# Performance work log

Measured on AMD Instinct MI355X. Metric: run time of the kernel, lower is better.

Reference implementation:

```python
import jax, jax.numpy as jnp
import numpy as np

B, N, C = 64, 197, 768
H = 12
N_TOK = 118
CUTOFF = 0.15


def setup_inputs() -> dict:
    key = jax.random.key(0)
    ks = jax.random.split(key, 6)
    s = 0.02
    return {
        "x": jax.random.normal(ks[0], (B, N, C), jnp.float32),
        "ln1_w": jnp.ones((C,), jnp.float32),
        "ln1_b": jnp.zeros((C,), jnp.float32),
        "qkv_w": jax.random.normal(ks[1], (3 * C, C), jnp.float32) * s,
        "proj_w": jax.random.normal(ks[2], (C, C), jnp.float32) * s,
        "proj_b": jnp.zeros((C,), jnp.float32),
        "gamma1": jnp.ones((C,), jnp.float32),
        "ln2_w": jnp.ones((C,), jnp.float32),
        "ln2_b": jnp.zeros((C,), jnp.float32),
        "fc1_w": jax.random.normal(ks[3], (4 * C, C), jnp.float32) * s,
        "fc1_b": jnp.zeros((4 * C,), jnp.float32),
        "fc2_w": jax.random.normal(ks[4], (C, 4 * C), jnp.float32) * s,
        "fc2_b": jnp.zeros((C,), jnp.float32),
        "gamma2": jnp.ones((C,), jnp.float32),
    }


def _ln(x, w, b, eps=1e-5):
    m = x.mean(-1, keepdims=True)
    v = ((x - m) ** 2).mean(-1, keepdims=True)
    return (x - m) / jnp.sqrt(v + eps) * w + b


def _attention(x, qkv_w, proj_w, proj_b):
    Bx, Nx, Cx = x.shape
    dh = Cx // H
    qkv = x @ qkv_w.T                                    # [B,N,3C]
    qk = qkv[:, :, : 2 * Cx].reshape(Bx, Nx, 2, H, dh).transpose(2, 0, 3, 1, 4)
    q, k = qk[0], qk[1]                                  # [B,H,N,dh]
    v = qkv[:, :, 2 * Cx :].reshape(Bx, Nx, H, dh).transpose(0, 2, 1, 3)
    attn = jax.nn.softmax((q * dh ** -0.5) @ k.transpose(0, 1, 3, 2), axis=-1)  # [B,H,N,N]
    out = (attn @ v).transpose(0, 2, 1, 3).reshape(Bx, Nx, Cx)
    return out @ proj_w.T + proj_b, attn


def _selector(x, attn, n_tokens, cutoff):
    # attention-weighted scores
    cls_aw = attn[:, :, 1:, 0].mean(-1)[..., None]        # [B,H,1]
    cls_attn = (attn[:, :, 0, 1:] * cls_aw).mean(1)       # [B,N-1]
    img_aw = attn[:, :, 0, 0][..., None]                  # [B,H,1]
    img_attn = (attn[:, :, 1:, 1:].mean(2) * img_aw).mean(1)
    token_attn = cls_attn + img_attn                      # [B,N-1]
    # FFT low-frequency-energy score (detached in original)
    img_token = jax.lax.stop_gradient(x[:, 1:].astype(jnp.float32).transpose(0, 2, 1))  # [B,C,N-1]
    f = jnp.fft.fft(img_token, axis=-1)
    amp = jnp.abs(f)
    pha = jnp.angle(f)
    L = img_token.shape[-1]
    d0 = (L * cutoff / 2.0) ** 2
    m0 = (L - 1) / 2.0
    grid = jnp.arange(L, dtype=jnp.float32)
    kernel = 1.0 - jnp.exp(-((grid - m0) ** 2) / (2.0 * d0))  # high-pass notch
    amp = amp * kernel
    f2 = amp * jnp.cos(pha) + 1j * amp * jnp.sin(pha)
    tok = jnp.fft.ifft(f2, axis=-1)                       # [B,C,N-1] complex
    token_lfe = jnp.abs(tok).sum(1) / jnp.abs(img_token).sum(1).mean(-1)[..., None]
    scores = token_lfe * token_attn                        # [B,N-1]
    _, idx = jax.lax.top_k(scores, n_tokens)               # [B,n_tokens]
    Cx = x.shape[-1]
    sav = jnp.take_along_axis(x[:, 1:], idx[:, :, None], axis=1)  # [B,n_tokens,C]
    return jnp.concatenate([x[:, 0:1], sav], axis=1)


def reference(x, ln1_w, ln1_b, qkv_w, proj_w, proj_b, gamma1,
              ln2_w, ln2_b, fc1_w, fc1_b, fc2_w, fc2_b, gamma2):
    x_msa, attn = _attention(_ln(x, ln1_w, ln1_b), qkv_w, proj_w, proj_b)
    x = gamma1 * x_msa + x
    x = _selector(x, attn, N_TOK, CUTOFF)                 # [B,1+N_TOK,C]
    h = _ln(x, ln2_w, ln2_b)
    h = jax.nn.gelu(h @ fc1_w.T + fc1_b, approximate=False)
    h = h @ fc2_w.T + fc2_b
    return gamma2 * h + x
```

## Files before the change

kernel.cpp:

```cpp
#include <hip/hip_runtime.h>
#include <math.h>

#define NTOK 197
#define NIMG 196
#define CDIM 768
#define NHEAD 12
#define HD 64
#define BATCH 64
#define NSEL 118
#define ROWS_FULL (BATCH*NTOK)
#define ROWS_SEL  (BATCH*(NSEL+1))

typedef short bf16x8 __attribute__((ext_vector_type(8)));
typedef float f32x4  __attribute__((ext_vector_type(4)));

#define GLDS(g, l) __builtin_amdgcn_global_load_lds( \
    (const __attribute__((address_space(1))) void*)(g), \
    (__attribute__((address_space(3))) void*)(l), 16, 0, 0)

__device__ __forceinline__ unsigned short f2bf(float f){
  union { float f; unsigned u; } v; v.f = f;
  unsigned r = v.u + 0x7FFF + ((v.u >> 16) & 1);
  return (unsigned short)(r >> 16);
}
__device__ __forceinline__ float bf2f(unsigned short h){
  union { unsigned u; float f; } v; v.u = ((unsigned)h) << 16; return v.f;
}

template<int OUT>
__global__ __launch_bounds__(256) void ln_kernel(
    const float* __restrict__ x, const float* __restrict__ w,
    const float* __restrict__ b, void* __restrict__ outv)
{
  const int row = blockIdx.x;
  const int t = threadIdx.x;
  const float* xr = x + (size_t)row * CDIM;
  float v0 = xr[t], v1 = xr[t+256], v2 = xr[t+512];
  float s = v0 + v1 + v2;
  __shared__ float red[4], red2[4];
  #pragma unroll
  for (int o=32;o>0;o>>=1) s += __shfl_down(s,o);
  if ((t&63)==0) red[t>>6] = s;
  __syncthreads();
  const float mean = (red[0]+red[1]+red[2]+red[3]) / 768.0f;
  const float d0=v0-mean, d1=v1-mean, d2=v2-mean;
  float vs = d0*d0 + d1*d1 + d2*d2;
  #pragma unroll
  for (int o=32;o>0;o>>=1) vs += __shfl_down(vs,o);
  if ((t&63)==0) red2[t>>6] = vs;
  __syncthreads();
  const float var = (red2[0]+red2[1]+red2[2]+red2[3]) / 768.0f;
  const float rstd = 1.0f / sqrtf(var + 1e-5f);
  const float o0 = d0*rstd*w[t]     + b[t];
  const float o1 = d1*rstd*w[t+256] + b[t+256];
  const float o2 = d2*rstd*w[t+512] + b[t+512];
  if (OUT == 0){
    float* orow = (float*)outv + (size_t)row * CDIM;
    orow[t] = o0; orow[t+256] = o1; orow[t+512] = o2;
  } else {
    unsigned short* orow = (unsigned short*)outv + (size_t)row * CDIM;
    orow[t] = f2bf(o0); orow[t+256] = f2bf(o1); orow[t+512] = f2bf(o2);
  }
}

__global__ __launch_bounds__(256) void ln_split3_kernel(
    const float* __restrict__ x, const float* __restrict__ w,
    const float* __restrict__ b, unsigned short* __restrict__ dst, size_t plane)
{
  const int row = blockIdx.x;
  const int t = threadIdx.x;
  const float* xr = x + (size_t)row * CDIM;
  float v0 = xr[t], v1 = xr[t+256], v2 = xr[t+512];
  float s = v0 + v1 + v2;
  __shared__ float red[4], red2[4];
  #pragma unroll
  for (int o=32;o>0;o>>=1) s += __shfl_down(s,o);
  if ((t&63)==0) red[t>>6] = s;
  __syncthreads();
  const float mean = (red[0]+red[1]+red[2]+red[3]) / 768.0f;
  const float d0=v0-mean, d1=v1-mean, d2=v2-mean;
  float vs = d0*d0 + d1*d1 + d2*d2;
  #pragma unroll
  for (int o=32;o>0;o>>=1) vs += __shfl_down(vs,o);
  if ((t&63)==0) red2[t>>6] = vs;
  __syncthreads();
  const float var = (red2[0]+red2[1]+red2[2]+red2[3]) / 768.0f;
  const float rstd = 1.0f / sqrtf(var + 1e-5f);
  const float ov[3] = { d0*rstd*w[t]     + b[t],
                        d1*rstd*w[t+256] + b[t+256],
                        d2*rstd*w[t+512] + b[t+512] };
  #pragma unroll
  for (int e=0;e<3;e++){
    const int col = t + e*256;
    const float f = ov[e];
    const unsigned short p0 = f2bf(f);
    const float r1 = f - bf2f(p0);
    const unsigned short p1 = f2bf(r1);
    const unsigned short p2 = f2bf(r1 - bf2f(p1));
    dst[(size_t)row*CDIM + col]             = p0;
    dst[plane + (size_t)row*CDIM + col]     = p1;
    dst[2*plane + (size_t)row*CDIM + col]   = p2;
  }
}

__global__ __launch_bounds__(256) void cvt_bf16_kernel(
    const float* __restrict__ src, unsigned short* __restrict__ dst, int n4)
{
  const int i = blockIdx.x*256 + threadIdx.x;
  if (i < n4){
    const float4 v = *(const float4*)(src + (size_t)i*4);
    dst[(size_t)i*4+0] = f2bf(v.x); dst[(size_t)i*4+1] = f2bf(v.y);
    dst[(size_t)i*4+2] = f2bf(v.z); dst[(size_t)i*4+3] = f2bf(v.w);
  }
}

__global__ __launch_bounds__(192) void cvt3_kernel(
    const float* __restrict__ w, unsigned short* __restrict__ W3, int K)
{
  const int n = blockIdx.x, t = threadIdx.x;
  const float4 v = *(const float4*)(w + (size_t)n*K + t*4);
  ushort4 hi, lo;
  hi.x = f2bf(v.x); lo.x = f2bf(v.x - bf2f(hi.x));
  hi.y = f2bf(v.y); lo.y = f2bf(v.y - bf2f(hi.y));
  hi.z = f2bf(v.z); lo.z = f2bf(v.z - bf2f(hi.z));
  hi.w = f2bf(v.w); lo.w = f2bf(v.w - bf2f(hi.w));
  *(ushort4*)(W3 + (size_t)n*2*K + t*4)     = hi;
  *(ushort4*)(W3 + (size_t)n*2*K + K + t*4) = lo;
}

__global__ __launch_bounds__(256) void cvt_split3_kernel(
    const float* __restrict__ src, unsigned short* __restrict__ dst,
    int n4, size_t plane)
{
  const int i = blockIdx.x*256 + threadIdx.x;
  if (i >= n4) return;
  const float4 v = *(const float4*)(src + (size_t)i*4);
  const float f[4] = {v.x, v.y, v.z, v.w};
  unsigned short p0[4], p1[4], p2[4];
  #pragma unroll
  for (int q=0;q<4;q++){
    p0[q] = f2bf(f[q]);
    const float r1 = f[q] - bf2f(p0[q]);
    p1[q] = f2bf(r1);
    const float r2 = r1 - bf2f(p1[q]);
    p2[q] = f2bf(r2);
  }
  *(ushort4*)(dst + (size_t)i*4)           = make_ushort4(p0[0],p0[1],p0[2],p0[3]);
  *(ushort4*)(dst + plane + (size_t)i*4)   = make_ushort4(p1[0],p1[1],p1[2],p1[3]);
  *(ushort4*)(dst + 2*plane + (size_t)i*4) = make_ushort4(p2[0],p2[1],p2[2],p2[3]);
}

__global__ __launch_bounds__(256) void gemm_f32_kernel(
    const float* __restrict__ A, const float* __restrict__ W,
    float* __restrict__ out, int M, int N, int K)
{
  __shared__ float As[16][132];
  __shared__ float Bs[16][132];
  const int t  = threadIdx.x;
  const int tx = t & 15, ty = t >> 4;
  const int m0 = blockIdx.x * 128, n0 = blockIdx.y * 128;
  const int lr = t >> 2, lc = (t & 3) << 2;
  float acc[2][2][4][4] = {{{{0.f}}}};
  const float4 z4 = make_float4(0.f,0.f,0.f,0.f);
  const int rowA0 = m0 + lr, rowA1 = m0 + 64 + lr;
  const size_t strA0 = (size_t)rowA0 * K, strA1 = (size_t)rowA1 * K;
  const size_t strW0 = (size_t)(n0+lr) * K, strW1 = (size_t)(n0+64+lr) * K;
  for (int k0=0; k0<K; k0+=16){
    float4 a0 = (rowA0 < M) ? *(const float4*)(A + strA0 + k0 + lc) : z4;
    float4 a1 = (rowA1 < M) ? *(const float4*)(A + strA1 + k0 + lc) : z4;
    float4 w0 = *(const float4*)(W + strW0 + k0 + lc);
    float4 w1 = *(const float4*)(W + strW1 + k0 + lc);
    __syncthreads();
    As[lc+0][lr]=a0.x; As[lc+1][lr]=a0.y; As[lc+2][lr]=a0.z; As[lc+3][lr]=a0.w;
    As[lc+0][64+lr]=a1.x; As[lc+1][64+lr]=a1.y; As[lc+2][64+lr]=a1.z; As[lc+3][64+lr]=a1.w;
    Bs[lc+0][lr]=w0.x; Bs[lc+1][lr]=w0.y; Bs[lc+2][lr]=w0.z; Bs[lc+3][lr]=w0.w;
    Bs[lc+0][64+lr]=w1.x; Bs[lc+1][64+lr]=w1.y; Bs[lc+2][64+lr]=w1.z; Bs[lc+3][64+lr]=w1.w;
    __syncthreads();
    #pragma unroll
    for (int k=0;k<16;k++){
      const float4 av0 = *(const float4*)&As[k][ty*4];
      const float4 av1 = *(const float4*)&As[k][64+ty*4];
      const float4 bv0 = *(const float4*)&Bs[k][tx*4];
      const float4 bv1 = *(const float4*)&Bs[k][64+tx*4];
      const float ar[2][4] = {{av0.x,av0.y,av0.z,av0.w},{av1.x,av1.y,av1.z,av1.w}};
      const float br[2][4] = {{bv0.x,bv0.y,bv0.z,bv0.w},{bv1.x,bv1.y,bv1.z,bv1.w}};
      #pragma unroll
      for (int ri=0;ri<2;ri++)
        #pragma unroll
        for (int i=0;i<4;i++)
          #pragma unroll
          for (int ci=0;ci<2;ci++)
            #pragma unroll
            for (int j=0;j<4;j++)
              acc[ri][ci][i][j] = fmaf(ar[ri][i], br[ci][j], acc[ri][ci][i][j]);
    }
  }
  #pragma unroll
  for (int ri=0;ri<2;ri++){
    #pragma unroll
    for (int i=0;i<4;i++){
      const int row = m0 + ri*64 + ty*4 + i;
      if (row >= M) continue;
      #pragma unroll
      for (int ci=0;ci<2;ci++){
        const int col = n0 + ci*64 + tx*4;
        *(float4*)(out + (size_t)row*N + col) =
          make_float4(acc[ri][ci][i][0],acc[ri][ci][i][1],acc[ri][ci][i][2],acc[ri][ci][i][3]);
      }
    }
  }
}

template<int EPI>
__global__ __launch_bounds__(256) void mfma_gemm_kernel(
    const unsigned short* __restrict__ A, const unsigned short* __restrict__ W,
    const float* __restrict__ bias, const float* __restrict__ gamma,
    const float* __restrict__ resid, void* __restrict__ outv,
    int M, int N, int K)
{
  __shared__ __align__(16) unsigned short As[128*64];
  __shared__ __align__(16) unsigned short Bs[128*64];
  const int t = threadIdx.x;
  const int w = t >> 6, lane = t & 63;
  const int m0 = blockIdx.x * 128, n0 = blockIdx.y * 128;
  const int wr = w >> 1, wc = w & 1;
  f32x4 acc[4][4];
  #pragma unroll
  for (int i=0;i<4;i++)
    #pragma unroll
    for (int j=0;j<4;j++){ acc[i][j][0]=0.f; acc[i][j][1]=0.f; acc[i][j][2]=0.f; acc[i][j][3]=0.f; }

  const int srow = lane >> 3;
  const int slot = lane & 7;
  const int scol = (slot ^ srow) * 8;
  const int rloc0 = w*32;
  const int fr = lane & 15;
  const int kg = lane >> 4;

  for (int k0 = 0; k0 < K; k0 += 64){
    __syncthreads();
    #pragma unroll
    for (int tt = 0; tt < 4; tt++){
      const int rl = rloc0 + tt*8;
      const int ra = rl + srow;
      GLDS(A + (size_t)(m0 + ra)*K + k0 + scol, As + rl*64);
      GLDS(W + (size_t)(n0 + ra)*K + k0 + scol, Bs + rl*64);
    }
    __syncthreads();
    #pragma unroll
    for (int ksub = 0; ksub < 2; ksub++){
      bf16x8 a[4], b[4];
      const int kbyte = ksub*64 + kg*16;
      #pragma unroll
      for (int mi=0; mi<4; mi++){
        const int ar = wr*64 + mi*16 + fr;
        a[mi] = *(const bf16x8*)(As + ar*64 + ((kbyte ^ ((ar&7)<<4)) >> 1));
      }
      #pragma unroll
      for (int ni=0; ni<4; ni++){
        const int br = wc*64 + ni*16 + fr;
        b[ni] = *(const bf16x8*)(Bs + br*64 + ((kbyte ^ ((br&7)<<4)) >> 1));
      }
      #pragma unroll
      for (int mi=0; mi<4; mi++)
        #pragma unroll
        for (int ni=0; ni<4; ni++)
          acc[mi][ni] = __builtin_amdgcn_mfma_f32_16x16x32_bf16(a[mi], b[ni], acc[mi][ni], 0, 0, 0);
    }
  }

  const int cL = lane & 15, rL = lane >> 4;
  #pragma unroll
  for (int mi=0; mi<4; mi++){
    #pragma unroll
    for (int ni=0; ni<4; ni++){
      const int col = n0 + wc*64 + ni*16 + cL;
      const int rowb = m0 + wr*64 + mi*16 + rL*4;
      const float bb = bias[col];
      #pragma unroll
      for (int r=0; r<4; r++){
        const int row = rowb + r;
        if (row >= M) continue;
        float v = acc[mi][ni][r] + bb;
        if (EPI == 2){
          v = 0.5f*v*(1.0f + erff(v*0.7071067811865475f));
          ((unsigned short*)outv)[(size_t)row*N + col] = f2bf(v);
        } else {
          v = gamma[col]*v + resid[(size_t)row*N + col];
          ((float*)outv)[(size_t)row*N + col] = v;
        }
      }
    }
  }
}

__global__ __launch_bounds__(512) void mfma_gemm6w_kernel(
    const unsigned short* __restrict__ A3, const unsigned short* __restrict__ W3,
    float* __restrict__ out, int M, int N, int K, size_t planeA, size_t planeW,
    int gx)
{
  __shared__ __align__(16) unsigned short As[3][64*64];
  __shared__ __align__(16) unsigned short Ws[256*64];
  const int nwg = gridDim.x;
  const int q8 = nwg >> 3, r8 = nwg & 7;
  const int xcd = blockIdx.x & 7, lid = blockIdx.x >> 3;
  const int swz = (xcd < r8) ? (xcd*(q8+1) + lid) : (r8*(q8+1) + (xcd-r8)*q8 + lid);
  const int bx = swz % gx, by = swz / gx;

  const int t = threadIdx.x;
  const int w = t >> 6, lane = t & 63;
  const int m0 = bx * 64, n0 = by * 256;
  const int wr = w >> 2, wc = w & 3;
  f32x4 acc[2][4];
  #pragma unroll
  for (int i=0;i<2;i++)
    #pragma unroll
    for (int j=0;j<4;j++){ acc[i][j][0]=0.f; acc[i][j][1]=0.f; acc[i][j][2]=0.f; acc[i][j][3]=0.f; }

  const int srow = lane >> 3;
  const int slot = lane & 7;
  const int scol = (slot ^ srow) * 8;
  const int aloc = w*8;
  const int wloc = w*32;
  const int fr = lane & 15;
  const int kg = lane >> 4;

  #define SEGW(NA)                                                            \
    _Pragma("unroll")                                                         \
    for (int ksub = 0; ksub < 2; ksub++){                                     \
      const int kbyte = ksub*64 + kg*16;                                      \
      bf16x8 b[4];                                                            \
      _Pragma("unroll")                                                       \
      for (int ni=0; ni<4; ni++){                                             \
        const int br = wc*64 + ni*16 + fr;                                    \
        b[ni] = *(const bf16x8*)(Ws + br*64 + ((kbyte ^ ((br&7)<<4)) >> 1));  \
      }                                                                       \
      _Pragma("unroll")                                                       \
      for (int p=0; p<NA; p++){                                               \
        bf16x8 a[2];                                                          \
        _Pragma("unroll")                                                     \
        for (int mi=0; mi<2; mi++){                                           \
          const int ar = wr*32 + mi*16 + fr;                                  \
          a[mi] = *(const bf16x8*)(As[p] + ar*64 + ((kbyte ^ ((ar&7)<<4)) >> 1)); \
        }                                                                     \
        _Pragma("unroll")                                                     \
        for (int mi=0; mi<2; mi++)                                            \
          _Pragma("unroll")                                                   \
          for (int ni=0; ni<4; ni++)                                          \
            acc[mi][ni] = __builtin_amdgcn_mfma_f32_16x16x32_bf16(a[mi], b[ni], acc[mi][ni], 0, 0, 0); \
      }                                                                       \
    }

  #define STAGE_W(P)                                                          \
    _Pragma("unroll")                                                         \
    for (int tt=0; tt<4; tt++){                                               \
      const int rl = wloc + tt*8;                                             \
      GLDS(W3 + (size_t)(P)*planeW + (size_t)(n0+rl+srow)*K + k0 + scol, Ws + rl*64); \
    }

  for (int k0 = 0; k0 < K; k0 += 64){
    __syncthreads();
    #pragma unroll
    for (int p=0; p<3; p++)
      GLDS(A3 + (size_t)p*planeA + (size_t)(m0+aloc+srow)*K + k0 + scol, As[p] + aloc*64);
    STAGE_W(0)
    __syncthreads();
    SEGW(3)
    __syncthreads();
    STAGE_W(1)
    __syncthreads();
    SEGW(2)
    __syncthreads();
    STAGE_W(2)
    __syncthreads();
    SEGW(1)
  }
  #undef SEGW
  #undef STAGE_W

  const int cL = lane & 15, rL = lane >> 4;
  #pragma unroll
  for (int mi=0; mi<2; mi++){
    #pragma unroll
    for (int ni=0; ni<4; ni++){
      const int col = n0 + wc*64 + ni*16 + cL;
      const int rowb = m0 + wr*32 + mi*16 + rL*4;
      #pragma unroll
      for (int r=0; r<4; r++){
        const int row = rowb + r;
        if (row >= M) continue;
        out[(size_t)row*N + col] = acc[mi][ni][r];
      }
    }
  }
}

__global__ __launch_bounds__(512) void mfma_proj3_kernel(
    const unsigned short* __restrict__ A, const unsigned short* __restrict__ W,
    const float* __restrict__ bias, const float* __restrict__ gamma,
    const float* __restrict__ resid, float* __restrict__ out,
    int M, int N, int K, int gx)
{
  __shared__ __align__(16) unsigned short Ah[64*64], Al[64*64];
  __shared__ __align__(16) unsigned short Ws[256*64];
  const int nwg = gridDim.x;
  const int q8 = nwg >> 3, r8 = nwg & 7;
  const int xcd = blockIdx.x & 7, lid = blockIdx.x >> 3;
  const int swz = (xcd < r8) ? (xcd*(q8+1) + lid) : (r8*(q8+1) + (xcd-r8)*q8 + lid);
  const int bx = swz % gx, by = swz / gx;

  const int t = threadIdx.x;
  const int w = t >> 6, lane = t & 63;
  const int m0 = bx * 64, n0 = by * 256;
  const int wr = w >> 2, wc = w & 3;
  const int lda = 2*K;
  f32x4 acc[2][4];
  #pragma unroll
  for (int i=0;i<2;i++)
    #pragma unroll
    for (int j=0;j<4;j++){ acc[i][j][0]=0.f; acc[i][j][1]=0.f; acc[i][j][2]=0.f; acc[i][j][3]=0.f; }

  const int srow = lane >> 3;
  const int slot = lane & 7;
  const int scol = (slot ^ srow) * 8;
  const int aloc = w*8;
  const int wloc = w*32;
  const int fr = lane & 15;
  const int kg = lane >> 4;

  #define PSEG(NA)                                                            \
    _Pragma("unroll")                                                         \
    for (int ksub = 0; ksub < 2; ksub++){                                     \
      const int kbyte = ksub*64 + kg*16;                                      \
      bf16x8 b[4];                                                            \
      _Pragma("unroll")                                                       \
      for (int ni=0; ni<4; ni++){                                             \
        const int br = wc*64 + ni*16 + fr;                                    \
        b[ni] = *(const bf16x8*)(Ws + br*64 + ((kbyte ^ ((br&7)<<4)) >> 1));  \
      }                                                                       \
      _Pragma("unroll")                                                       \
      for (int mi=0; mi<2; mi++){                                             \
        const int ar = wr*32 + mi*16 + fr;                                    \
        const int ao = ar*64 + ((kbyte ^ ((ar&7)<<4)) >> 1);                  \
        bf16x8 ah = *(const bf16x8*)(Ah + ao);                                \
        _Pragma("unroll")                                                     \
        for (int ni=0; ni<4; ni++)                                            \
          acc[mi][ni] = __builtin_amdgcn_mfma_f32_16x16x32_bf16(ah, b[ni], acc[mi][ni], 0, 0, 0); \
        if (NA > 1){                                                          \
          bf16x8 al = *(const bf16x8*)(Al + ao);                              \
          _Pragma("unroll")                                                   \
          for (int ni=0; ni<4; ni++)                                          \
            acc[mi][ni] = __builtin_amdgcn_mfma_f32_16x16x32_bf16(al, b[ni], acc[mi][ni], 0, 0, 0); \
        }                                                                     \
      }                                                                       \
    }

  for (int k0 = 0; k0 < K; k0 += 64){
    __syncthreads();
    {
      const size_t abase = (size_t)(m0+aloc+srow)*lda + k0 + scol;
      GLDS(A + abase,     Ah + aloc*64);
      GLDS(A + abase + K, Al + aloc*64);
    }
    #pragma unroll
    for (int tt=0; tt<4; tt++){
      const int rl = wloc + tt*8;
      GLDS(W + (size_t)(n0+rl+srow)*lda + k0 + scol, Ws + rl*64);
    }
    __syncthreads();
    PSEG(2)
    __syncthreads();
    #pragma unroll
    for (int tt=0; tt<4; tt++){
      const int rl = wloc + tt*8;
      GLDS(W + (size_t)(n0+rl+srow)*lda + K + k0 + scol, Ws + rl*64);
    }
    __syncthreads();
    PSEG(1)
  }
  #undef PSEG

  const int cL = lane & 15, rL = lane >> 4;
  #pragma unroll
  for (int mi=0; mi<2; mi++){
    #pragma unroll
    for (int ni=0; ni<4; ni++){
      const int col = n0 + wc*64 + ni*16 + cL;
      const int rowb = m0 + wr*32 + mi*16 + rL*4;
      const float bb = bias[col];
      const float gg = gamma[col];
      #pragma unroll
      for (int r=0; r<4; r++){
        const int row = rowb + r;
        if (row >= M) continue;
        out[(size_t)row*N + col] = gg*(acc[mi][ni][r] + bb) + resid[(size_t)row*N + col];
      }
    }
  }
}

__global__ __launch_bounds__(256) void attn_stats_kernel(
    const float* __restrict__ qkv, double* __restrict__ mbuf, double* __restrict__ lbuf)
{
  __shared__ float Kt[NTOK][HD];
  __shared__ double q0s[HD];
  __shared__ float m0sh;
  __shared__ double red[4];
  const int bh = blockIdx.x;
  const int b = bh / NHEAD, h = bh % NHEAD;
  const float* basep = qkv + (size_t)b*NTOK*2304 + h*HD;
  for (int li=threadIdx.x; li<NTOK*16; li+=256){
    const int r = li >> 4, c4 = (li & 15) << 2;
    *(float4*)&Kt[r][c4] = *(const float4*)(basep + (size_t)r*2304 + 768 + c4);
  }
  if (threadIdx.x < 16){
    const float4 t4 = *(const float4*)(basep + threadIdx.x*4);
    q0s[threadIdx.x*4+0] = (double)t4.x*0.125; q0s[threadIdx.x*4+1] = (double)t4.y*0.125;
    q0s[threadIdx.x*4+2] = (double)t4.z*0.125; q0s[threadIdx.x*4+3] = (double)t4.w*0.125;
  }
  __syncthreads();
  const int i = threadIdx.x;
  if (i < NTOK){
    float4 q[16];
    #pragma unroll
    for (int dd=0; dd<16; dd++){
      float4 tq = *(const float4*)(basep + (size_t)i*2304 + dd*4);
      q[dd] = make_float4(tq.x*0.125f, tq.y*0.125f, tq.z*0.125f, tq.w*0.125f);
    }
    float m = -INFINITY, l = 0.f;
    for (int j=0;j<NTOK;j++){
      float s = 0.f;
      #pragma unroll
      for (int dd=0;dd<16;dd++){
        const float4 kk = *(const float4*)&Kt[j][dd*4];
        s = fmaf(q[dd].x,kk.x,s); s = fmaf(q[dd].y,kk.y,s);
        s = fmaf(q[dd].z,kk.z,s); s = fmaf(q[dd].w,kk.w,s);
      }
      const float mn = fmaxf(m, s);
      l = l*expf(m-mn) + expf(s-mn);
      m = mn;
    }
    mbuf[bh*NTOK+i] = (double)m;
    if (i > 0) lbuf[bh*NTOK+i] = (double)(1.0f/l);
    if (i == 0) m0sh = m;
  }
  __syncthreads();
  double e = 0.0;
  if (i < NTOK){
    double s64 = 0.0;
    #pragma unroll
    for (int d=0; d<HD; d++) s64 = fma(q0s[d], (double)Kt[i][d], s64);
    e = exp(s64 - (double)m0sh);
  }
  #pragma unroll
  for (int o=32;o>0;o>>=1) e += __shfl_down(e,o);
  if ((i&63)==0) red[i>>6] = e;
  __syncthreads();
  if (i==0) lbuf[bh*NTOK] = 1.0/(red[0]+red[1]+red[2]+red[3]);
}

__global__ __launch_bounds__(256) void attn_pv_kernel(
    const float* __restrict__ qkv, const double* __restrict__ mbuf,
    const double* __restrict__ lbuf, unsigned short* __restrict__ msa3)
{
  __shared__ float Kt[NTOK][HD];
  __shared__ float Vt[NTOK][HD];
  const int bh = blockIdx.x;
  const int b = bh / NHEAD, h = bh % NHEAD;
  const float* basep = qkv + (size_t)b*NTOK*2304 + h*HD;
  for (int li=threadIdx.x; li<NTOK*16; li+=256){
    const int r = li >> 4, c4 = (li & 15) << 2;
    *(float4*)&Kt[r][c4] = *(const float4*)(basep + (size_t)r*2304 +  768 + c4);
    *(float4*)&Vt[r][c4] = *(const float4*)(basep + (size_t)r*2304 + 1536 + c4);
  }
  __syncthreads();
  const int i = threadIdx.x;
  if (i >= NTOK) return;
  float4 q[16];
  #pragma unroll
  for (int dd=0; dd<16; dd++){
    float4 tq = *(const float4*)(basep + (size_t)i*2304 + dd*4);
    q[dd] = make_float4(tq.x*0.125f, tq.y*0.125f, tq.z*0.125f, tq.w*0.125f);
  }
  const float m    = (float)mbuf[bh*NTOK + i];
  const float linv = (float)lbuf[bh*NTOK + i];
  float4 o[16];
  #pragma unroll
  for (int dd=0;dd<16;dd++) o[dd] = make_float4(0.f,0.f,0.f,0.f);
  for (int j=0;j<NTOK;j++){
    float s = 0.f;
    #pragma unroll
    for (int dd=0;dd<16;dd++){
      const float4 kk = *(const float4*)&Kt[j][dd*4];
      s = fmaf(q[dd].x,kk.x,s); s = fmaf(q[dd].y,kk.y,s);
      s = fmaf(q[dd].z,kk.z,s); s = fmaf(q[dd].w,kk.w,s);
    }
    const float p = expf(s - m) * linv;
    #pragma unroll
    for (int dd=0;dd<16;dd++){
      const float4 vv = *(const float4*)&Vt[j][dd*4];
      o[dd].x = fmaf(p,vv.x,o[dd].x); o[dd].y = fmaf(p,vv.y,o[dd].y);
      o[dd].z = fmaf(p,vv.z,o[dd].z); o[dd].w = fmaf(p,vv.w,o[dd].w);
    }
  }
  unsigned short* orow = msa3 + ((size_t)b*NTOK + i)*1536 + h*HD;
  #pragma unroll
  for (int dd=0;dd<16;dd++){
    const float4 v = o[dd];
    ushort4 hi, lo;
    hi.x = f2bf(v.x); lo.x = f2bf(v.x - bf2f(hi.x));
    hi.y = f2bf(v.y); lo.y = f2bf(v.y - bf2f(hi.y));
    hi.z = f2bf(v.z); lo.z = f2bf(v.z - bf2f(hi.z));
    hi.w = f2bf(v.w); lo.w = f2bf(v.w - bf2f(hi.w));
    *(ushort4*)(orow + dd*4)       = hi;
    *(ushort4*)(orow + 768 + dd*4) = lo;
  }
}

__global__ __launch_bounds__(256) void attn_sel_kernel(
    const float* __restrict__ qkv, const double* __restrict__ mbuf,
    const double* __restrict__ lbuf, double* __restrict__ ta_part)
{
  __shared__ float Qt[NTOK][HD];
  __shared__ double q0s[HD];
  __shared__ float msf[NTOK], lsf[NTOK];
  __shared__ double m0d, l0inv;
  __shared__ double sh_cs0, sh_r00;
  const int bh = blockIdx.x;
  const int b = bh / NHEAD, h = bh % NHEAD;
  const float* basep = qkv + (size_t)b*NTOK*2304 + h*HD;
  for (int li=threadIdx.x; li<NTOK*16; li+=256){
    const int r = li >> 4, c4 = (li & 15) << 2;
    float4 tq = *(const float4*)(basep + (size_t)r*2304 + c4);
    Qt[r][c4+0]=tq.x*0.125f; Qt[r][c4+1]=tq.y*0.125f;
    Qt[r][c4+2]=tq.z*0.125f; Qt[r][c4+3]=tq.w*0.125f;
  }
  if (threadIdx.x < 16){
    const float4 t4 = *(const float4*)(basep + threadIdx.x*4);
    q0s[threadIdx.x*4+0] = (double)t4.x*0.125; q0s[threadIdx.x*4+1] = (double)t4.y*0.125;
    q0s[threadIdx.x*4+2] = (double)t4.z*0.125; q0s[threadIdx.x*4+3] = (double)t4.w*0.125;
  }
  for (int li=threadIdx.x; li<NTOK; li+=256){
    msf[li] = (float)mbuf[bh*NTOK+li];
    lsf[li] = (float)lbuf[bh*NTOK+li];
  }
  if (threadIdx.x == 0){ m0d = mbuf[bh*NTOK]; l0inv = lbuf[bh*NTOK]; }
  __syncthreads();
  const int j = threadIdx.x;
  double colsum = 0.0, row0 = 0.0;
  if (j < NTOK){
    float4 kreg[16];
    #pragma unroll
    for (int dd=0;dd<16;dd++) kreg[dd] = *(const float4*)(basep + (size_t)j*2304 + 768 + dd*4);
    {
      double s64 = 0.0;
      #pragma unroll
      for (int dd=0;dd<16;dd++){
        s64 = fma(q0s[dd*4+0], (double)kreg[dd].x, s64);
        s64 = fma(q0s[dd*4+1], (double)kreg[dd].y, s64);
        s64 = fma(q0s[dd*4+2], (double)kreg[dd].z, s64);
        s64 = fma(q0s[dd*4+3], (double)kreg[dd].w, s64);
      }
      row0 = exp(s64 - m0d) * l0inv;
    }
    for (int i2=1;i2<NTOK;i2++){
      float s = 0.f;
      #pragma unroll
      for (int dd=0;dd<16;dd++){
        const float4 qq = *(const float4*)&Qt[i2][dd*4];
        s = fmaf(qq.x,kreg[dd].x,s); s = fmaf(qq.y,kreg[dd].y,s);
        s = fmaf(qq.z,kreg[dd].z,s); s = fmaf(qq.w,kreg[dd].w,s);
      }
      colsum += (double)(expf(s - msf[i2]) * lsf[i2]);
    }
  }
  if (j == 0){ sh_cs0 = colsum; sh_r00 = row0; }
  __syncthreads();
  if (j >= 1 && j < NTOK){
    ta_part[(size_t)bh*NIMG + (j-1)] = row0 * (sh_cs0 / 196.0) + (colsum / 196.0) * sh_r00;
  }
}

__global__ __launch_bounds__(256) void reduce_ta_kernel(
    const double* __restrict__ ta_part, double* __restrict__ token_attn)
{
  const int b = blockIdx.x, j = threadIdx.x;
  if (j < NIMG){
    double s = 0.0;
    for (int h=0; h<NHEAD; h++) s += ta_part[((size_t)b*NHEAD + h)*NIMG + j];
    token_attn[b*NIMG + j] = s / 12.0;
  }
}

__global__ __launch_bounds__(256) void circ_kernel(float* __restrict__ circ)
{
  const int d = blockIdx.x;
  const int g = threadIdx.x;
  __shared__ double rs[4], is[4];
  double re = 0.0, im = 0.0;
  if (g < NIMG){
    const double d0   = (196.0 * 0.15 / 2.0);
    const double twod = 2.0 * d0 * d0;
    const double gg = (double)g - 97.5;
    const double kg = 1.0 - exp(-(gg*gg)/twod);
    const int gd = (g*d) % NIMG;
    const double ang = 6.283185307179586476925286766559 * ((double)gd / 196.0);
    re = kg * cos(ang);
    im = kg * sin(ang);
  }
  #pragma unroll
  for (int o=32;o>0;o>>=1){ re += __shfl_down(re,o); im += __shfl_down(im,o); }
  if ((g&63)==0){ rs[g>>6] = re; is[g>>6] = im; }
  __syncthreads();
  if (g == 0){
    circ[d]        = (float)((rs[0]+rs[1]+rs[2]+rs[3]) / 196.0);
    circ[NIMG + d] = (float)((is[0]+is[1]+is[2]+is[3]) / 196.0);
  }
}

__global__ __launch_bounds__(256) void lfe_kernel(
    const float* __restrict__ x1, const float* __restrict__ circ,
    double* __restrict__ lfe_part, double* __restrict__ den_part)
{
  __shared__ float xs[NIMG][36];
  __shared__ float2 c2[NIMG];
  __shared__ double red[4];
  const int cg = blockIdx.x, b = blockIdx.y;
  const int c0 = cg * 32;
  for (int li=threadIdx.x; li<NIMG*32; li+=256){
    const int m = li >> 5, ch = li & 31;
    xs[m][ch] = x1[((size_t)b*NTOK + 1 + m)*CDIM + c0 + ch];
  }
  for (int li=threadIdx.x; li<NIMG; li+=256) c2[li] = make_float2(circ[li], circ[NIMG+li]);
  __syncthreads();
  const int n = threadIdx.x;
  double lfe_sum = 0.0, den_sum = 0.0;
  if (n < NIMG){
    #pragma unroll 1
    for (int g=0; g<4; g++){
      const int cc0 = g*8;
      float re[8] = {0,0,0,0,0,0,0,0};
      float im[8] = {0,0,0,0,0,0,0,0};
      int d = n;
      for (int mm=0; mm<NIMG; mm++){
        const float2 cc = c2[d];
        const float4 xa = *(const float4*)&xs[mm][cc0];
        const float4 xb = *(const float4*)&xs[mm][cc0+4];
        const float xv[8] = {xa.x,xa.y,xa.z,xa.w,xb.x,xb.y,xb.z,xb.w};
        #pragma unroll
        for (int q=0;q<8;q++){
          re[q] = fmaf(cc.x, xv[q], re[q]);
          im[q] = fmaf(cc.y, xv[q], im[q]);
        }
        d = (d==0) ? (NIMG-1) : (d-1);
      }
      #pragma unroll
      for (int q=0;q<8;q++) lfe_sum += (double)sqrtf(re[q]*re[q] + im[q]*im[q]);
    }
    #pragma unroll
    for (int q=0;q<8;q++){
      const float4 xv = *(const float4*)&xs[n][q*4];
      den_sum += (double)fabsf(xv.x)+(double)fabsf(xv.y)+(double)fabsf(xv.z)+(double)fabsf(xv.w);
    }
    lfe_part[((size_t)b*24 + cg)*NIMG + n] = lfe_sum;
  }
  double s = (n < NIMG) ? den_sum : 0.0;
  #pragma unroll
  for (int o=32;o>0;o>>=1) s += __shfl_down(s,o);
  if ((threadIdx.x & 63) == 0) red[threadIdx.x >> 6] = s;
  __syncthreads();
  if (threadIdx.x == 0) den_part[b*24 + cg] = red[0]+red[1]+red[2]+red[3];
}

__global__ __launch_bounds__(256) void scores_kernel(
    const double* __restrict__ lfe_part, const double* __restrict__ den_part,
    const double* __restrict__ token_attn, double* __restrict__ scores)
{
  const int b = blockIdx.x, n = threadIdx.x;
  if (n < NIMG){
    double num = 0.0;
    for (int cg=0; cg<24; cg++) num += lfe_part[((size_t)b*24 + cg)*NIMG + n];
    double den = 0.0;
    for (int cg=0; cg<24; cg++) den += den_part[b*24 + cg];
    const double tl = num / (den / 196.0);
    scores[b*NIMG + n] = tl * token_attn[b*NIMG + n];
  }
}

__global__ void topk_kernel(const double* __restrict__ scores, int* __restrict__ idx)
{
  __shared__ double w[NIMG];
  const int b = blockIdx.x, lane = threadIdx.x;
  for (int i=lane; i<NIMG; i+=64) w[i] = scores[b*NIMG + i];
  __syncthreads();
  for (int r=0; r<NSEL; r++){
    double bv = -INFINITY; int bi = NIMG;
    for (int i=lane; i<NIMG; i+=64){
      const double v = w[i];
      if (v > bv){ bv = v; bi = i; }
    }
    #pragma unroll
    for (int o=32;o>0;o>>=1){
      const double ov = __shfl_down(bv,o);
      const int    oi = __shfl_down(bi,o);
      if (ov > bv || (ov == bv && oi < bi)){ bv = ov; bi = oi; }
    }
    if (lane == 0){
      idx[b*NSEL + r] = bi;
      w[bi] = -INFINITY;
    }
    __syncthreads();
  }
}

__global__ void gather_kernel(const float* __restrict__ x1, const int* __restrict__ idx,
                              float* __restrict__ xsel)
{
  const int row = blockIdx.x;
  const int b = row / (NSEL+1), r = row % (NSEL+1);
  const int src = (r == 0) ? 0 : (1 + idx[b*NSEL + (r-1)]);
  const float4* s = (const float4*)(x1 + ((size_t)b*NTOK + src)*CDIM);
  float4* d = (float4*)(xsel + (size_t)row*CDIM);
  d[threadIdx.x] = s[threadIdx.x];
}

extern "C" void kernel_launch(void* const* d_in, const int* in_sizes, int n_in,
                              void* d_out, int out_size, void* d_ws, size_t ws_size,
                              hipStream_t stream)
{
  const float* x      = (const float*)d_in[0];
  const float* ln1_w  = (const float*)d_in[1];
  const float* ln1_b  = (const float*)d_in[2];
  const float* qkv_w  = (const float*)d_in[3];
  const float* proj_w = (const float*)d_in[4];
  const float* proj_b = (const float*)d_in[5];
  const float* gamma1 = (const float*)d_in[6];
  const float* ln2_w  = (const float*)d_in[7];
  const float* ln2_b  = (const float*)d_in[8];
  const float* fc1_w  = (const float*)d_in[9];
  const float* fc1_b  = (const float*)d_in[10];
  const float* fc2_w  = (const float*)d_in[11];
  const float* fc2_b  = (const float*)d_in[12];
  const float* gamma2 = (const float*)d_in[13];
  float* out = (float*)d_out;
  float* ws  = (float*)d_ws;

  float* R1 = ws;
  float* R2 = ws + 9732096;
  double* D = (double*)(ws + 9732096 + 29048832);
  double* mbuf = D;
  double* lbuf = mbuf + 151296;
  double* tap  = lbuf + 151296;
  double* ta   = tap  + 150528;
  double* lfep = ta   + 12544;
  double* denp = lfep + 301056;
  double* sc   = denp + 1536;
  float* circ  = (float*)(sc + 12544);
  int*   idxb  = (int*)(circ + 392);
  unsigned short* W3p = (unsigned short*)(ws + 40350472);
  unsigned short* WQ3 = (unsigned short*)(ws + 40940296);
  unsigned short* XQ3 = (unsigned short*)(ws + 43594504);
  const size_t NEED_BYTES = (size_t)58192648 * 4;

  float* xln  = R1;
  unsigned short* msa3 = (unsigned short*)R1;
  float* xsel = R1;
  float* qkv  = R2;
  float* x1   = R2;
  unsigned short* ln2o_bf = (unsigned short*)(R2 + 9682944);
  unsigned short* fc1w_bf = (unsigned short*)(R2 + 12632064);
  unsigned short* fc2w_bf = (unsigned short*)(R2 + 13811712);
  unsigned short* h1_bf   = (unsigned short*)(R2 + 14991360);

  if (ws_size >= NEED_BYTES){
    ln_split3_kernel<<<ROWS_FULL, 256, 0, stream>>>(x, ln1_w, ln1_b, XQ3, (size_t)9732096);
    cvt_split3_kernel<<<(442368+255)/256, 256, 0, stream>>>(qkv_w, WQ3, 442368, (size_t)1769472);
    mfma_gemm6w_kernel<<<197*9, 512, 0, stream>>>(XQ3, WQ3, qkv, ROWS_FULL, 2304, 768,
                                                  (size_t)9732096, (size_t)1769472, 197);
  } else {
    ln_kernel<0><<<ROWS_FULL, 256, 0, stream>>>(x, ln1_w, ln1_b, xln);
    gemm_f32_kernel<<<dim3(99,18), 256, 0, stream>>>(xln, qkv_w, qkv, ROWS_FULL, 2304, 768);
  }
  attn_stats_kernel<<<BATCH*NHEAD, 256, 0, stream>>>(qkv, mbuf, lbuf);
  attn_pv_kernel<<<BATCH*NHEAD, 256, 0, stream>>>(qkv, mbuf, lbuf, msa3);
  attn_sel_kernel<<<BATCH*NHEAD, 256, 0, stream>>>(qkv, mbuf, lbuf, tap);
  reduce_ta_kernel<<<BATCH, 256, 0, stream>>>(tap, ta);
  cvt3_kernel<<<CDIM, 192, 0, stream>>>(proj_w, W3p, CDIM);
  mfma_proj3_kernel<<<197*3, 512, 0, stream>>>(msa3, W3p, proj_b, gamma1, x,
                                               x1, ROWS_FULL, CDIM, CDIM, 197);
  cvt_bf16_kernel<<<2304, 256, 0, stream>>>(fc1_w, fc1w_bf, 589824);
  cvt_bf16_kernel<<<2304, 256, 0, stream>>>(fc2_w, fc2w_bf, 589824);
  circ_kernel<<<NIMG, 256, 0, stream>>>(circ);
  lfe_kernel<<<dim3(24, BATCH), 256, 0, stream>>>(x1, circ, lfep, denp);
  scores_kernel<<<BATCH, 256, 0, stream>>>(lfep, denp, ta, sc);
  topk_kernel<<<BATCH, 64, 0, stream>>>(sc, idxb);
  gather_kernel<<<ROWS_SEL, 192, 0, stream>>>(x1, idxb, xsel);
  ln_kernel<1><<<ROWS_SEL, 256, 0, stream>>>(xsel, ln2_w, ln2_b, ln2o_bf);
  mfma_gemm_kernel<2><<<dim3(60,24), 256, 0, stream>>>(ln2o_bf, fc1w_bf, fc1_b, nullptr,
                                                       nullptr, h1_bf, ROWS_SEL, 3072, 768);
  mfma_gemm_kernel<3><<<dim3(60,6), 256, 0, stream>>>(h1_bf, fc2w_bf, fc2_b, gamma2,
                                                      xsel, out, ROWS_SEL, 768, 3072);
}
```

Measured before the change: 1.367 ms.

## Fuse attention stats and PV kernels; retile MLP GEMMs to 64x256 with XCD swizzle

Merges the attention softmax-statistics kernel and the PV kernel into one, so K is loaded into shared memory once and the per-row max and normaliser stay in registers instead of round-tripping through global memory. The MLP GEMMs move from 128x128 tiles with 256 threads to 64x256 tiles with 512 threads and an XCD-aware block swizzle. The swizzle keeps blocks that share weight tiles on the same XCD, and the smaller M tile wastes less work on the partial last row tile (M=7616). The fused attention kernel uses more shared memory per block, which may lower occupancy.

```diff
diff --git a/kernel.cpp b/kernel.cpp
--- a/kernel.cpp
+++ b/kernel.cpp
@@ -206,89 +206,6 @@
         const int col = n0 + ci*64 + tx*4;
         *(float4*)(out + (size_t)row*N + col) =
           make_float4(acc[ri][ci][i][0],acc[ri][ci][i][1],acc[ri][ci][i][2],acc[ri][ci][i][3]);
-      }
-    }
-  }
-}
-
-template<int EPI>
-__global__ __launch_bounds__(256) void mfma_gemm_kernel(
-    const unsigned short* __restrict__ A, const unsigned short* __restrict__ W,
-    const float* __restrict__ bias, const float* __restrict__ gamma,
-    const float* __restrict__ resid, void* __restrict__ outv,
-    int M, int N, int K)
-{
-  __shared__ __align__(16) unsigned short As[128*64];
-  __shared__ __align__(16) unsigned short Bs[128*64];
-  const int t = threadIdx.x;
-  const int w = t >> 6, lane = t & 63;
-  const int m0 = blockIdx.x * 128, n0 = blockIdx.y * 128;
-  const int wr = w >> 1, wc = w & 1;
-  f32x4 acc[4][4];
-  #pragma unroll
-  for (int i=0;i<4;i++)
-    #pragma unroll
-    for (int j=0;j<4;j++){ acc[i][j][0]=0.f; acc[i][j][1]=0.f; acc[i][j][2]=0.f; acc[i][j][3]=0.f; }
-
-  const int srow = lane >> 3;
-  const int slot = lane & 7;
-  const int scol = (slot ^ srow) * 8;
-  const int rloc0 = w*32;
-  const int fr = lane & 15;
-  const int kg = lane >> 4;
-
-  for (int k0 = 0; k0 < K; k0 += 64){
-    __syncthreads();
-    #pragma unroll
-    for (int tt = 0; tt < 4; tt++){
-      const int rl = rloc0 + tt*8;
-      const int ra = rl + srow;
-      GLDS(A + (size_t)(m0 + ra)*K + k0 + scol, As + rl*64);
-      GLDS(W + (size_t)(n0 + ra)*K + k0 + scol, Bs + rl*64);
-    }
-    __syncthreads();
-    #pragma unroll
-    for (int ksub = 0; ksub < 2; ksub++){
-      bf16x8 a[4], b[4];
-      const int kbyte = ksub*64 + kg*16;
-      #pragma unroll
-      for (int mi=0; mi<4; mi++){
-        const int ar = wr*64 + mi*16 + fr;
-        a[mi] = *(const bf16x8*)(As + ar*64 + ((kbyte ^ ((ar&7)<<4)) >> 1));
-      }
-      #pragma unroll
-      for (int ni=0; ni<4; ni++){
-        const int br = wc*64 + ni*16 + fr;
-        b[ni] = *(const bf16x8*)(Bs + br*64 + ((kbyte ^ ((br&7)<<4)) >> 1));
-      }
-      #pragma unroll
-      for (int mi=0; mi<4; mi++)
-        #pragma unroll
-        for (int ni=0; ni<4; ni++)
-          acc[mi][ni] = __builtin_amdgcn_mfma_f32_16x16x32_bf16(a[mi], b[ni], acc[mi][ni], 0, 0, 0);
-    }
-  }
-
-  const int cL = lane & 15, rL = lane >> 4;
-  #pragma unroll
-  for (int mi=0; mi<4; mi++){
-    #pragma unroll
-    for (int ni=0; ni<4; ni++){
-      const int col = n0 + wc*64 + ni*16 + cL;
-      const int rowb = m0 + wr*64 + mi*16 + rL*4;
-      const float bb = bias[col];
-      #pragma unroll
-      for (int r=0; r<4; r++){
-        const int row = rowb + r;
-        if (row >= M) continue;
-        float v = acc[mi][ni][r] + bb;
-        if (EPI == 2){
-          v = 0.5f*v*(1.0f + erff(v*0.7071067811865475f));
-          ((unsigned short*)outv)[(size_t)row*N + col] = f2bf(v);
-        } else {
-          v = gamma[col]*v + resid[(size_t)row*N + col];
-          ((float*)outv)[(size_t)row*N + col] = v;
-        }
       }
     }
   }
@@ -390,6 +307,96 @@
         const int row = rowb + r;
         if (row >= M) continue;
         out[(size_t)row*N + col] = acc[mi][ni][r];
+      }
+    }
+  }
+}
+
+template<int EPI>
+__global__ __launch_bounds__(512) void mfma_gemm1w_kernel(
+    const unsigned short* __restrict__ A, const unsigned short* __restrict__ W,
+    const float* __restrict__ bias, const float* __restrict__ gamma,
+    const float* __restrict__ resid, void* __restrict__ outv,
+    int M, int N, int K, int gx)
+{
+  __shared__ __align__(16) unsigned short As[64*64];
+  __shared__ __align__(16) unsigned short Ws[256*64];
+  const int nwg = gridDim.x;
+  const int q8 = nwg >> 3, r8 = nwg & 7;
+  const int xcd = blockIdx.x & 7, lid = blockIdx.x >> 3;
+  const int swz = (xcd < r8) ? (xcd*(q8+1) + lid) : (r8*(q8+1) + (xcd-r8)*q8 + lid);
+  const int bx = swz % gx, by = swz / gx;
+
+  const int t = threadIdx.x;
+  const int w = t >> 6, lane = t & 63;
+  const int m0 = bx * 64, n0 = by * 256;
+  const int wr = w >> 2, wc = w & 3;
+  f32x4 acc[2][4];
+  #pragma unroll
+  for (int i=0;i<2;i++)
+    #pragma unroll
+    for (int j=0;j<4;j++){ acc[i][j][0]=0.f; acc[i][j][1]=0.f; acc[i][j][2]=0.f; acc[i][j][3]=0.f; }
+
+  const int srow = lane >> 3;
+  const int slot = lane & 7;
+  const int scol = (slot ^ srow) * 8;
+  const int aloc = w*8;
+  const int wloc = w*32;
+  const int fr = lane & 15;
+  const int kg = lane >> 4;
+
+  for (int k0 = 0; k0 < K; k0 += 64){
+    __syncthreads();
+    GLDS(A + (size_t)(m0+aloc+srow)*K + k0 + scol, As + aloc*64);
+    #pragma unroll
+    for (int tt=0; tt<4; tt++){
+      const int rl = wloc + tt*8;
+      GLDS(W + (size_t)(n0+rl+srow)*K + k0 + scol, Ws + rl*64);
+    }
+    __syncthreads();
+    #pragma unroll
+    for (int ksub = 0; ksub < 2; ksub++){
+      const int kbyte = ksub*64 + kg*16;
+      bf16x8 b[4];
+      #pragma unroll
+      for (int ni=0; ni<4; ni++){
+        const int br = wc*64 + ni*16 + fr;
+        b[ni] = *(const bf16x8*)(Ws + br*64 + ((kbyte ^ ((br&7)<<4)) >> 1));
+      }
+      bf16x8 a[2];
+      #pragma unroll
+      for (int mi=0; mi<2; mi++){
+        const int ar = wr*32 + mi*16 + fr;
+        a[mi] = *(const bf16x8*)(As + ar*64 + ((kbyte ^ ((ar&7)<<4)) >> 1));
+      }
+      #pragma unroll
+      for (int mi=0; mi<2; mi++)
+        #pragma unroll
+        for (int ni=0; ni<4; ni++)
+          acc[mi][ni] = __builtin_amdgcn_mfma_f32_16x16x32_bf16(a[mi], b[ni], acc[mi][ni], 0, 0, 0);
+    }
+  }
+
+  const int cL = lane & 15, rL = lane >> 4;
+  #pragma unroll
+  for (int mi=0; mi<2; mi++){
+    #pragma unroll
+    for (int ni=0; ni<4; ni++){
+      const int col = n0 + wc*64 + ni*16 + cL;
+      const int rowb = m0 + wr*32 + mi*16 + rL*4;
+      const float bb = bias[col];
+      #pragma unroll
+      for (int r=0; r<4; r++){
+        const int row = rowb + r;
+        if (row >= M) continue;
+        float v = acc[mi][ni][r] + bb;
+        if (EPI == 2){
+          v = 0.5f*v*(1.0f + erff(v*0.7071067811865475f));
+          ((unsigned short*)outv)[(size_t)row*N + col] = f2bf(v);
+        } else {
+          v = gamma[col]*v + resid[(size_t)row*N + col];
+          ((float*)outv)[(size_t)row*N + col] = v;
+        }
       }
     }
   }
@@ -499,72 +506,16 @@
   }
 }
 
-__global__ __launch_bounds__(256) void attn_stats_kernel(
-    const float* __restrict__ qkv, double* __restrict__ mbuf, double* __restrict__ lbuf)
+__global__ __launch_bounds__(256) void attn_fused_kernel(
+    const float* __restrict__ qkv, double* __restrict__ mbuf,
+    double* __restrict__ lbuf, unsigned short* __restrict__ msa3)
 {
   __shared__ float Kt[NTOK][HD];
+  __shared__ float Vt[NTOK][HD];
   __shared__ double q0s[HD];
   __shared__ float m0sh;
   __shared__ double red[4];
-  const int bh = blockIdx.x;
-  const int b = bh / NHEAD, h = bh % NHEAD;
-  const float* basep = qkv + (size_t)b*NTOK*2304 + h*HD;
-  for (int li=threadIdx.x; li<NTOK*16; li+=256){
-    const int r = li >> 4, c4 = (li & 15) << 2;
-    *(float4*)&Kt[r][c4] = *(const float4*)(basep + (size_t)r*2304 + 768 + c4);
-  }
-  if (threadIdx.x < 16){
-    const float4 t4 = *(const float4*)(basep + threadIdx.x*4);
-    q0s[threadIdx.x*4+0] = (double)t4.x*0.125; q0s[threadIdx.x*4+1] = (double)t4.y*0.125;
-    q0s[threadIdx.x*4+2] = (double)t4.z*0.125; q0s[threadIdx.x*4+3] = (double)t4.w*0.125;
-  }
-  __syncthreads();
-  const int i = threadIdx.x;
-  if (i < NTOK){
-    float4 q[16];
-    #pragma unroll
-    for (int dd=0; dd<16; dd++){
-      float4 tq = *(const float4*)(basep + (size_t)i*2304 + dd*4);
-      q[dd] = make_float4(tq.x*0.125f, tq.y*0.125f, tq.z*0.125f, tq.w*0.125f);
-    }
-    float m = -INFINITY, l = 0.f;
-    for (int j=0;j<NTOK;j++){
-      float s = 0.f;
-      #pragma unroll
-      for (int dd=0;dd<16;dd++){
-        const float4 kk = *(const float4*)&Kt[j][dd*4];
-        s = fmaf(q[dd].x,kk.x,s); s = fmaf(q[dd].y,kk.y,s);
-        s = fmaf(q[dd].z,kk.z,s); s = fmaf(q[dd].w,kk.w,s);
-      }
-      const float mn = fmaxf(m, s);
-      l = l*expf(m-mn) + expf(s-mn);
-      m = mn;
-    }
-    mbuf[bh*NTOK+i] = (double)m;
-    if (i > 0) lbuf[bh*NTOK+i] = (double)(1.0f/l);
-    if (i == 0) m0sh = m;
-  }
-  __syncthreads();
-  double e = 0.0;
-  if (i < NTOK){
-    double s64 = 0.0;
-    #pragma unroll
-    for (int d=0; d<HD; d++) s64 = fma(q0s[d], (double)Kt[i][d], s64);
-    e = exp(s64 - (double)m0sh);
-  }
-  #pragma unroll
-  for (int o=32;o>0;o>>=1) e += __shfl_down(e,o);
-  if ((i&63)==0) red[i>>6] = e;
-  __syncthreads();
-  if (i==0) lbuf[bh*NTOK] = 1.0/(red[0]+red[1]+red[2]+red[3]);
-}
-
-__global__ __launch_bounds__(256) void attn_pv_kernel(
-    const float* __restrict__ qkv, const double* __restrict__ mbuf,
-    const double* __restrict__ lbuf, unsigned short* __restrict__ msa3)
-{
-  __shared__ float Kt[NTOK][HD];
-  __shared__ float Vt[NTOK][HD];
+  __shared__ float l0f;
   const int bh = blockIdx.x;
   const int b = bh / NHEAD, h = bh % NHEAD;
   const float* basep = qkv + (size_t)b*NTOK*2304 + h*HD;
@@ -573,17 +524,59 @@
     *(float4*)&Kt[r][c4] = *(const float4*)(basep + (size_t)r*2304 +  768 + c4);
     *(float4*)&Vt[r][c4] = *(const float4*)(basep + (size_t)r*2304 + 1536 + c4);
   }
+  if (threadIdx.x < 16){
+    const float4 t4 = *(const float4*)(basep + threadIdx.x*4);
+    q0s[threadIdx.x*4+0] = (double)t4.x*0.125; q0s[threadIdx.x*4+1] = (double)t4.y*0.125;
+    q0s[threadIdx.x*4+2] = (double)t4.z*0.125; q0s[threadIdx.x*4+3] = (double)t4.w*0.125;
+  }
   __syncthreads();
   const int i = threadIdx.x;
+  float4 q[16];
+  float m = -INFINITY, linv = 0.f;
+  if (i < NTOK){
+    #pragma unroll
+    for (int dd=0; dd<16; dd++){
+      float4 tq = *(const float4*)(basep + (size_t)i*2304 + dd*4);
+      q[dd] = make_float4(tq.x*0.125f, tq.y*0.125f, tq.z*0.125f, tq.w*0.125f);
+    }
+    float l = 0.f;
+    for (int j=0;j<NTOK;j++){
+      float s = 0.f;
+      #pragma unroll
+      for (int dd=0;dd<16;dd++){
+        const float4 kk = *(const float4*)&Kt[j][dd*4];
+        s = fmaf(q[dd].x,kk.x,s); s = fmaf(q[dd].y,kk.y,s);
+        s = fmaf(q[dd].z,kk.z,s); s = fmaf(q[dd].w,kk.w,s);
+      }
+      const float mn = fmaxf(m, s);
+      l = l*expf(m-mn) + expf(s-mn);
+      m = mn;
+    }
+    mbuf[bh*NTOK+i] = (double)m;
+    linv = 1.0f/l;
+    if (i > 0) lbuf[bh*NTOK+i] = (double)linv;
+    if (i == 0) m0sh = m;
+  }
+  __syncthreads();
+  double e = 0.0;
+  if (i < NTOK){
+    double s64 = 0.0;
+    #pragma unroll
+    for (int d=0; d<HD; d++) s64 = fma(q0s[d], (double)Kt[i][d], s64);
+    e = exp(s64 - (double)m0sh);
+  }
+  #pragma unroll
+  for (int o=32;o>0;o>>=1) e += __shfl_down(e,o);
+  if ((i&63)==0) red[i>>6] = e;
+  __syncthreads();
+  if (i==0){
+    const double l0 = 1.0/(red[0]+red[1]+red[2]+red[3]);
+    lbuf[bh*NTOK] = l0;
+    l0f = (float)l0;
+  }
+  __syncthreads();
   if (i >= NTOK) return;
-  float4 q[16];
-  #pragma unroll
-  for (int dd=0; dd<16; dd++){
-    float4 tq = *(const float4*)(basep + (size_t)i*2304 + dd*4);
-    q[dd] = make_float4(tq.x*0.125f, tq.y*0.125f, tq.z*0.125f, tq.w*0.125f);
-  }
-  const float m    = (float)mbuf[bh*NTOK + i];
-  const float linv = (float)lbuf[bh*NTOK + i];
+  if (i == 0) linv = l0f;
   float4 o[16];
   #pragma unroll
   for (int dd=0;dd<16;dd++) o[dd] = make_float4(0.f,0.f,0.f,0.f);
@@ -881,8 +874,7 @@
     ln_kernel<0><<<ROWS_FULL, 256, 0, stream>>>(x, ln1_w, ln1_b, xln);
     gemm_f32_kernel<<<dim3(99,18), 256, 0, stream>>>(xln, qkv_w, qkv, ROWS_FULL, 2304, 768);
   }
-  attn_stats_kernel<<<BATCH*NHEAD, 256, 0, stream>>>(qkv, mbuf, lbuf);
-  attn_pv_kernel<<<BATCH*NHEAD, 256, 0, stream>>>(qkv, mbuf, lbuf, msa3);
+  attn_fused_kernel<<<BATCH*NHEAD, 256, 0, stream>>>(qkv, mbuf, lbuf, msa3);
   attn_sel_kernel<<<BATCH*NHEAD, 256, 0, stream>>>(qkv, mbuf, lbuf, tap);
   reduce_ta_kernel<<<BATCH, 256, 0, stream>>>(tap, ta);
   cvt3_kernel<<<CDIM, 192, 0, stream>>>(proj_w, W3p, CDIM);
@@ -896,8 +888,8 @@
   topk_kernel<<<BATCH, 64, 0, stream>>>(sc, idxb);
   gather_kernel<<<ROWS_SEL, 192, 0, stream>>>(x1, idxb, xsel);
   ln_kernel<1><<<ROWS_SEL, 256, 0, stream>>>(xsel, ln2_w, ln2_b, ln2o_bf);
-  mfma_gemm_kernel<2><<<dim3(60,24), 256, 0, stream>>>(ln2o_bf, fc1w_bf, fc1_b, nullptr,
-                                                       nullptr, h1_bf, ROWS_SEL, 3072, 768);
-  mfma_gemm_kernel<3><<<dim3(60,6), 256, 0, stream>>>(h1_bf, fc2w_bf, fc2_b, gamma2,
-                                                      xsel, out, ROWS_SEL, 768, 3072);
-}
+  mfma_gemm1w_kernel<2><<<119*12, 512, 0, stream>>>(ln2o_bf, fc1w_bf, fc1_b, nullptr,
+                                                    nullptr, h1_bf, ROWS_SEL, 3072, 768, 119);
+  mfma_gemm1w_kernel<3><<<119*3, 512, 0, stream>>>(h1_bf, fc2w_bf, fc2_b, gamma2,
+                                                   xsel, out, ROWS_SEL, 768, 3072, 119);
+}
```

Result: slower. 1.395 ms (+2.1%).
